# Kernel tuning notes

Measured on AMD Instinct MI355X. Metric: run time of the kernel, lower is better.

Reference implementation:

```python
import jax, jax.numpy as jnp
import numpy as np

N, E, H, G, L = 50000, 640000, 128, 8, 3

def setup_inputs() -> dict:
    key = jax.random.key(0)
    ks = jax.random.split(key, 10)
    s = 1.0 / np.sqrt(H)
    return {
        "x": jax.random.normal(ks[0], (N, H), jnp.float32),
        "query": jax.random.normal(ks[1], (G, H), jnp.float32),
        "Wl": jax.random.normal(ks[2], (L, H, H), jnp.float32) * s,
        "bl": jax.random.normal(ks[3], (L, H), jnp.float32) * s,
        "Wr": jax.random.normal(ks[4], (L, H, H), jnp.float32) * s,
        "Wlin": jax.random.normal(ks[5], (H, H), jnp.float32) * s,
        "blin": jax.random.normal(ks[6], (H,), jnp.float32) * s,
        "edge_index": jax.random.randint(ks[7], (2, E), 0, N, jnp.int64),
        "batch_vec": jnp.sort(jax.random.randint(ks[8], (N,), 0, G, jnp.int64)),
    }

def reference(x, query, Wl, bl, Wr, Wlin, blin, edge_index, batch_vec):
    src, dst = edge_index[0], edge_index[1]
    n = x.shape[0]
    for i in range(L):
        # SAGEConv(aggr='max'): gather neighbor feats, scatter-max to dst
        m = jax.ops.segment_max(x[src], dst, num_segments=n)  # [N,H]
        m = jnp.where(jnp.isfinite(m), m, 0.0)  # isolated nodes -> 0 (PyG)
        x = jax.nn.relu(m @ Wl[i].T + bl[i] + x @ Wr[i].T)
    x = x @ Wlin.T + blin  # encoder final linear
    # cosine scoring per graph, vectorized via batch_vec
    xn = x / jnp.linalg.norm(x, axis=1, keepdims=True).clip(1e-12)
    qn = query / jnp.linalg.norm(query, axis=1, keepdims=True).clip(1e-12)
    scores = jnp.sum(xn * qn[batch_vec], axis=1)  # [N]
    return scores
```

## Files before the change

### kernel.cpp

```cpp
#include <hip/hip_runtime.h>
#include <math.h>

#define H 128
#define NBUCK_MAX 256

typedef _Float16 half8 __attribute__((ext_vector_type(8)));
typedef float f32x16 __attribute__((ext_vector_type(16)));
typedef int int4v __attribute__((ext_vector_type(4)));

__device__ __forceinline__ half8 h8max(half8 a, half8 b) {
#if defined(__has_builtin) && __has_builtin(__builtin_elementwise_max)
    return __builtin_elementwise_max(a, b);
#else
    half8 r;
#pragma unroll
    for (int j = 0; j < 8; ++j) r[j] = a[j] > b[j] ? a[j] : b[j];
    return r;
#endif
}

__device__ __forceinline__ half8 h8shfl_xor(half8 v, int mask) {
    int4v iv;
    __builtin_memcpy(&iv, &v, 16);
#pragma unroll
    for (int j = 0; j < 4; ++j) iv[j] = __shfl_xor(iv[j], mask, 64);
    half8 r;
    __builtin_memcpy(&r, &iv, 16);
    return r;
}


__global__ __launch_bounds__(256) void prep_all(
    const int* __restrict__ ei, int E, int* __restrict__ blockhist, int NB,
    const float* __restrict__ x, const float* __restrict__ query,
    const float* __restrict__ Wl, const float* __restrict__ Wr,
    const float* __restrict__ Wlin, _Float16* __restrict__ xh,
    _Float16* __restrict__ wimg, float* __restrict__ qn, int n8, int HB, int SB,
    int WB) {
    int b = blockIdx.x;
    int tid = threadIdx.x;
    if (b < HB) {
        __shared__ int hist[NBUCK_MAX];
        for (int j = tid; j < NB; j += 256) hist[j] = 0;
        __syncthreads();
        int base = b * 2048 + tid;
#pragma unroll
        for (int k = 0; k < 8; ++k) {
            int e = base + k * 256;
            if (e < E) atomicAdd(&hist[ei[E + e] >> 8], 1);
        }
        __syncthreads();
        for (int j = tid; j < NB; j += 256) blockhist[(size_t)b * NB + j] = hist[j];
    } else if (b < HB + SB) {
        int i = (b - HB) * 256 + tid;
        if (i < n8) {
            const float4* x4 = (const float4*)x;
            float4 u = x4[(size_t)i * 2], v = x4[(size_t)i * 2 + 1];
            float f[8] = {u.x, u.y, u.z, u.w, v.x, v.y, v.z, v.w};
            half8 h;
#pragma unroll
            for (int j = 0; j < 8; ++j) h[j] = (_Float16)f[j];
            *(half8*)(xh + (size_t)i * 8) = h;
        }
    } else if (b < HB + SB + WB) {
        int gidx = (b - HB - SB) * 256 + tid;
        if (gidx < 7 * 2048) {
            int mat = gidx / 2048;
            int rem = gidx - mat * 2048;
            int kc4 = rem >> 9;
            int r2 = rem & 511;
            int s = r2 >> 6;
            int lane = r2 & 63;
            int ks = s >> 2;
            int colgrp = s & 3;
            int lhi = lane >> 5, l31 = lane & 31;
            int n = colgrp * 32 + l31;
            int g16 = kc4 * 4 + ks * 2 + lhi;
            const float* src = (mat == 6) ? Wlin
                             : ((mat & 1) ? Wr + (mat >> 1) * H * H
                                          : Wl + (mat >> 1) * H * H);
            const float* p = src + n * H + g16 * 8;
            half8 h, l;
#pragma unroll
            for (int j = 0; j < 8; ++j) {
                float v = p[j];
                _Float16 hh = (_Float16)v;
                h[j] = hh;
                l[j] = (_Float16)(v - (float)hh);
            }
            size_t base = (size_t)mat * 32768 + (size_t)kc4 * 8192 +
                          (size_t)s * 1024 + (size_t)lane * 16;
            *(half8*)(wimg + base) = h;
            *(half8*)(wimg + base + 8) = l;
        }
    } else {
        int g = b - HB - SB - WB;
        __shared__ float part[4];
        float v = (tid < 128) ? query[g * H + tid] : 0.f;
        float ss = v * v;
#pragma unroll
        for (int off = 32; off > 0; off >>= 1) ss += __shfl_xor(ss, off, 64);
        if ((tid & 63) == 0) part[tid >> 6] = ss;
        __syncthreads();
        float tot = part[0] + part[1];
        if (tid < 128) qn[g * H + tid] = v / fmaxf(sqrtf(tot), 1e-12f);
    }
}


__global__ __launch_bounds__(512) void scan_hist(int* __restrict__ blockhist,
                                                 int HB, int NB,
                                                 int* __restrict__ coltot) {
    __shared__ int buf[512];
    int j = blockIdx.x;
    int tid = threadIdx.x;
    int carry = 0;
    for (int base = 0; base < HB; base += 512) {
        int t = base + tid;
        int v = (t < HB) ? blockhist[(size_t)t * NB + j] : 0;
        buf[tid] = v;
        __syncthreads();
        int incl = v;
#pragma unroll
        for (int off = 1; off < 512; off <<= 1) {
            int u = (tid >= off) ? buf[tid - off] : 0;
            __syncthreads();
            incl += u;
            buf[tid] = incl;
            __syncthreads();
        }
        if (t < HB) blockhist[(size_t)t * NB + j] = carry + incl - v;
        carry += buf[511];
        __syncthreads();
    }
    if (tid == 0) coltot[j] = carry;
}


__global__ __launch_bounds__(256) void scan_buckets(const int* __restrict__ coltot,
                                                    int NB,
                                                    int* __restrict__ colstart) {
    __shared__ int buf[256];
    int tid = threadIdx.x;
    int v = (tid < NB) ? coltot[tid] : 0;
    buf[tid] = v;
    __syncthreads();
    int incl = v;
#pragma unroll
    for (int off = 1; off < 256; off <<= 1) {
        int u = (tid >= off) ? buf[tid - off] : 0;
        __syncthreads();
        incl += u;
        buf[tid] = incl;
        __syncthreads();
    }
    if (tid < NB) colstart[tid] = incl - v;
}


__global__ __launch_bounds__(256) void scatter_edges(
    const int* __restrict__ ei, int E, const int* __restrict__ blockhist,
    const int* __restrict__ colstart, int NB, int2* __restrict__ bucketed) {
    __shared__ int sbase[NBUCK_MAX];
    __shared__ int scnt[NBUCK_MAX];
    int b = blockIdx.x;
    int tid = threadIdx.x;
    for (int j = tid; j < NB; j += 256) {
        sbase[j] = colstart[j] + blockhist[(size_t)b * NB + j];
        scnt[j] = 0;
    }
    __syncthreads();
    int base = b * 2048 + tid;
#pragma unroll
    for (int k = 0; k < 8; ++k) {
        int e = base + k * 256;
        if (e < E) {
            int s = ei[e];
            int d = ei[E + e];
            int bu = d >> 8;
            int r = atomicAdd(&scnt[bu], 1);
            bucketed[sbase[bu] + r] = make_int2(d, s);
        }
    }
}


__global__ __launch_bounds__(256) void build_rows(
    const int2* __restrict__ bucketed, const int* __restrict__ colstart,
    const int* __restrict__ coltot, int* __restrict__ deg,
    int* __restrict__ adjp32, int* __restrict__ govf, int* __restrict__ ovf,
    int N) {
    __shared__ __align__(16) int rows[256 * 32];
    __shared__ int cnt[256];
    int k = blockIdx.x;
    int tid = threadIdx.x;
    cnt[tid] = 0;
    for (int j = tid; j < 256 * 32; j += 256) rows[j] = 0;
    __syncthreads();

    int s0 = colstart[k];
    int cn = coltot[k];
    for (int i = tid; i < cn; i += 256) {
        int2 rec = bucketed[s0 + i];
        int dl = rec.x & 255;
        int sl = atomicAdd(&cnt[dl], 1);
        if (sl < 32) {
            rows[dl * 32 + sl] = rec.y;
        } else {
            int o = atomicAdd(govf, 1);
            ovf[2 * o] = rec.x;
            ovf[2 * o + 1] = rec.y;
        }
    }
    __syncthreads();
    int node0 = k << 8;
    if (node0 + tid < N) deg[node0 + tid] = cnt[tid];
    for (int j = tid; j < 2048; j += 256) {
        int row = j >> 3, q = j & 7;
        int node = node0 + row;
        if (node < N)
            ((int4*)adjp32)[(size_t)node * 8 + q] = ((const int4*)rows)[row * 8 + q];
    }
}


template <bool FINAL_UNUSED>
__global__ __launch_bounds__(512, 8) void layer_fused(
    const half8* __restrict__ Xh, const int* __restrict__ deg,
    const int* __restrict__ adjp32, const int* __restrict__ ovf,
    const int* __restrict__ ovfcnt, const _Float16* __restrict__ Bimg,
    const float* __restrict__ bias, _Float16* __restrict__ Yh, int N) {
    __shared__ __align__(16) unsigned char smem[16384];
    _Float16* sU = (_Float16*)smem;
    _Float16* sX = (_Float16*)(smem + 8192);
    float* comb = (float*)smem;

    int tid = threadIdx.x;
    int w = tid >> 6;
    int wq = w & 3;
    int wh = w >> 2;
    int lane = tid & 63;
    int l31 = lane & 31;
    int lhi = lane >> 5;
    int n0 = blockIdx.x * 32;

    const half8 hz = {(_Float16)0.f, (_Float16)0.f, (_Float16)0.f, (_Float16)0.f,
                      (_Float16)0.f, (_Float16)0.f, (_Float16)0.f, (_Float16)0.f};

    {
        int row = tid >> 4;
        int g = tid & 15;
        int nn = n0 + row;
        half8 h = hz;
        if (nn < N) h = Xh[(size_t)nn * 16 + g];
        *(half8*)&sX[row * 128 + ((g ^ (row & 15)) << 3)] = h;
    }

    {
        int sub = lane >> 4;
        int lf = lane & 15;
        int nd4 = n0 + w * 4;
        int node = nd4 + sub;
        int nodec = node < N ? node : N - 1;
        int degv = (node < N) ? deg[node] : 0;

        int dmx = degv;
        {
            int t = __shfl_xor(dmx, 16, 64);
            dmx = t > dmx ? t : dmx;
            t = __shfl_xor(dmx, 32, 64);
            dmx = t > dmx ? t : dmx;
        }

        int r0 = adjp32[(size_t)nodec * 32 + lf];
        int r1 = 0;
        if (dmx > 16) r1 = adjp32[(size_t)nodec * 32 + 16 + lf];
#pragma unroll
        for (int i = 0; i < 4; ++i) {
            int d = __shfl(degv, i << 4, 64);
            int base = i << 4;
            int j0 = sub, j1 = 4 + sub, j2 = 8 + sub, j3 = 12 + sub;
            int i0 = __shfl(r0, base | (j0 < d ? j0 : 0), 64);
            int i1 = __shfl(r0, base | (j1 < d ? j1 : 0), 64);
            int i2 = __shfl(r0, base | (j2 < d ? j2 : 0), 64);
            int i3 = __shfl(r0, base | (j3 < d ? j3 : 0), 64);
            half8 v0 = Xh[(size_t)i0 * 16 + lf];
            half8 v1 = Xh[(size_t)i1 * 16 + lf];
            half8 v2 = Xh[(size_t)i2 * 16 + lf];
            half8 v3 = Xh[(size_t)i3 * 16 + lf];
            half8 acc = h8max(h8max(v0, v1), h8max(v2, v3));
            if (d > 16) {
                int k4 = (16 + sub) < d ? sub : 0;
                int k5 = (20 + sub) < d ? 4 + sub : 0;
                int k6 = (24 + sub) < d ? 8 + sub : 0;
                int k7 = (28 + sub) < d ? 12 + sub : 0;
                int i4 = __shfl(r1, base | k4, 64);
                int i5 = __shfl(r1, base | k5, 64);
                int i6 = __shfl(r1, base | k6, 64);
                int i7 = __shfl(r1, base | k7, 64);
                half8 u0 = Xh[(size_t)i4 * 16 + lf];
                half8 u1 = Xh[(size_t)i5 * 16 + lf];
                half8 u2 = Xh[(size_t)i6 * 16 + lf];
                half8 u3 = Xh[(size_t)i7 * 16 + lf];
                acc = h8max(acc, h8max(h8max(u0, u1), h8max(u2, u3)));
            }
            if (d > 32) {
                int cntv = ovfcnt[0];
                for (int kk = 0; kk < cntv; ++kk) {
                    if (ovf[2 * kk] == nd4 + i) {
                        half8 u = Xh[(size_t)ovf[2 * kk + 1] * 16 + lf];
                        acc = h8max(acc, u);
                    }
                }
            }
            acc = h8max(acc, h8shfl_xor(acc, 16));
            acc = h8max(acc, h8shfl_xor(acc, 32));
            if (d == 0) acc = hz;
            int row = w * 4 + i;
            if (sub == 0) *(half8*)&sU[row * 128 + ((lf ^ (row & 15)) << 3)] = acc;
        }
    }
    __syncthreads();

    f32x16 acc;
    int col = wq * 32 + l31;
    {
        float b0 = (wh == 0) ? bias[col] : 0.f;
#pragma unroll
        for (int r = 0; r < 16; ++r) acc[r] = b0;
    }

    int rl = l31;
    const _Float16* A = wh ? sX : sU;
    const _Float16* B = Bimg + (size_t)wh * 32768;

#pragma unroll
    for (int kc4 = 0; kc4 < 4; ++kc4) {
#pragma unroll
        for (int ks = 0; ks < 2; ++ks) {
            int g16 = kc4 * 4 + ks * 2 + lhi;
            int posA = g16 ^ (rl & 15);
            half8 ah = *(const half8*)&A[rl * 128 + posA * 8];
            size_t boff =
                (size_t)kc4 * 8192 + (size_t)(ks * 4 + wq) * 1024 + (size_t)lane * 16;
            half8 bh = *(const half8*)&B[boff];
            half8 bl2 = *(const half8*)&B[boff + 8];
            acc = __builtin_amdgcn_mfma_f32_32x32x16_f16(ah, bh, acc, 0, 0, 0);
            acc = __builtin_amdgcn_mfma_f32_32x32x16_f16(ah, bl2, acc, 0, 0, 0);
        }
    }

    __syncthreads();

    if (wh == 1) {
#pragma unroll
        for (int r = 0; r < 16; ++r) {
            int rloc = (r & 3) + 8 * (r >> 2) + 4 * lhi;
            comb[wq * 1024 + rloc * 32 + l31] = acc[r];
        }
    }
    __syncthreads();

    if (wh == 0) {
#pragma unroll
        for (int r = 0; r < 16; ++r) {
            int rloc = (r & 3) + 8 * (r >> 2) + 4 * lhi;
            float y = acc[r] + comb[wq * 1024 + rloc * 32 + l31];
            int row = n0 + rloc;
            if (row < N) Yh[(size_t)row * H + col] = (_Float16)fmaxf(y, 0.f);
        }
    }
}


__global__ __launch_bounds__(256) void final_mfma6(
    const half8* __restrict__ Xh, const _Float16* __restrict__ Bimg,
    const float* __restrict__ blin, const float* __restrict__ qn,
    const int* __restrict__ bv, float* __restrict__ out, int N) {
    __shared__ __align__(16) _Float16 sA[4096];

    int tid = threadIdx.x;
    int w = tid >> 6;
    int lane = tid & 63;
    int l31 = lane & 31;
    int lhi = lane >> 5;
    int n0 = blockIdx.x * 32;

    {
        const half8 hz = {(_Float16)0.f, (_Float16)0.f, (_Float16)0.f, (_Float16)0.f,
                          (_Float16)0.f, (_Float16)0.f, (_Float16)0.f, (_Float16)0.f};
#pragma unroll
        for (int t = 0; t < 2; ++t) {
            int idx = tid + t * 256;
            int row = idx >> 4;
            int g = idx & 15;
            int nn = n0 + row;
            half8 h = hz;
            if (nn < N) h = Xh[(size_t)nn * 16 + g];
            *(half8*)&sA[row * 128 + ((g ^ (row & 15)) << 3)] = h;
        }
    }

    int arow = n0 + l31;
    arow = arow < N ? arow : N - 1;
    int gl = bv[arow];

    f32x16 acc;
    int col = w * 32 + l31;
    {
        float b = blin[col];
#pragma unroll
        for (int r = 0; r < 16; ++r) acc[r] = b;
    }
    int rl = l31;
    __syncthreads();

#pragma unroll
    for (int kc4 = 0; kc4 < 4; ++kc4) {
#pragma unroll
        for (int ks = 0; ks < 2; ++ks) {
            int g16 = kc4 * 4 + ks * 2 + lhi;
            int posA = g16 ^ (rl & 15);
            half8 ah = *(const half8*)&sA[rl * 128 + posA * 8];
            size_t boff =
                (size_t)kc4 * 8192 + (size_t)(ks * 4 + w) * 1024 + (size_t)lane * 16;
            half8 bh = *(const half8*)&Bimg[boff];
            half8 bl2 = *(const half8*)&Bimg[boff + 8];
            acc = __builtin_amdgcn_mfma_f32_32x32x16_f16(ah, bh, acc, 0, 0, 0);
            acc = __builtin_amdgcn_mfma_f32_32x32x16_f16(ah, bl2, acc, 0, 0, 0);
        }
    }

    __syncthreads();
    float* sP = (float*)sA;
#pragma unroll
    for (int r = 0; r < 16; ++r) {
        int rloc = (r & 3) + 8 * (r >> 2) + 4 * lhi;
        int g = __shfl(gl, rloc, 32);
        float y = acc[r];
        float q = qn[(size_t)g * H + col];
        float ss = y * y;
        float sd = y * q;
#pragma unroll
        for (int off = 1; off <= 16; off <<= 1) {
            ss += __shfl_xor(ss, off, 64);
            sd += __shfl_xor(sd, off, 64);
        }
        if (l31 == 0) {
            sP[(rloc * 4 + w) * 2] = ss;
            sP[(rloc * 4 + w) * 2 + 1] = sd;
        }
    }
    __syncthreads();
    if (tid < 32) {
        int row = n0 + tid;
        if (row < N) {
            float ss = 0.f, sd = 0.f;
#pragma unroll
            for (int q = 0; q < 4; ++q) {
                ss += sP[(tid * 4 + q) * 2];
                sd += sP[(tid * 4 + q) * 2 + 1];
            }
            out[row] = sd / fmaxf(sqrtf(ss), 1e-12f);
        }
    }
}


extern "C" void kernel_launch(void* const* d_in, const int* in_sizes, int n_in,
                              void* d_out, int out_size, void* d_ws, size_t ws_size,
                              hipStream_t stream) {
    const float* x = (const float*)d_in[0];
    const float* query = (const float*)d_in[1];
    const float* Wl = (const float*)d_in[2];
    const float* bl = (const float*)d_in[3];
    const float* Wr = (const float*)d_in[4];
    const float* Wlin = (const float*)d_in[5];
    const float* blin = (const float*)d_in[6];
    const int* ei = (const int*)d_in[7];
    const int* bv = (const int*)d_in[8];
    float* out = (float*)d_out;

    const int N = in_sizes[0] / H;
    const int E = in_sizes[7] / 2;
    const int G = in_sizes[1] / H;

    const int HB = (E + 2047) / 2048;
    const int NB = (N + 255) >> 8;

    char* p = (char*)d_ws;
    auto alloc = [&](size_t bytes) {
        char* r = p;
        p += (bytes + 255) & ~(size_t)255;
        return r;
    };
    int* deg = (int*)alloc((size_t)(N + 1) * sizeof(int));
    int* govf = deg + N;
    int* adjp32 = (int*)alloc((size_t)N * 32 * sizeof(int));
    int* ovf = (int*)alloc((size_t)E * 2 * sizeof(int));
    int* blockhist = (int*)alloc((size_t)HB * NB * sizeof(int));
    int* colstart = (int*)alloc((size_t)NB * sizeof(int));
    int* coltot = (int*)alloc((size_t)NB * sizeof(int));
    int2* bucketed = (int2*)alloc((size_t)E * sizeof(int2));
    float* qn = (float*)alloc((size_t)G * H * sizeof(float));
    _Float16* wimg = (_Float16*)alloc((size_t)7 * 32768 * sizeof(_Float16));
    size_t actH = (size_t)N * H * sizeof(_Float16);
    _Float16* xah = (_Float16*)alloc(actH);
    _Float16* xbh = (_Float16*)alloc(actH);

    hipMemsetAsync(govf, 0, sizeof(int), stream);

    const int n8 = N * H / 8;
    const int SB = (n8 + 255) / 256;
    const int WB = (7 * 2048 + 255) / 256;
    prep_all<<<HB + SB + WB + G, 256, 0, stream>>>(ei, E, blockhist, NB, x,
                                                   query, Wl, Wr, Wlin, xah,
                                                   wimg, qn, n8, HB, SB, WB);
    scan_hist<<<NB, 512, 0, stream>>>(blockhist, HB, NB, coltot);
    scan_buckets<<<1, 256, 0, stream>>>(coltot, NB, colstart);
    scatter_edges<<<HB, 256, 0, stream>>>(ei, E, blockhist, colstart, NB,
                                          bucketed);
    build_rows<<<NB, 256, 0, stream>>>(bucketed, colstart, coltot, deg, adjp32,
                                       govf, ovf, N);

    const int NGm = (N + 31) / 32;

    layer_fused<false><<<NGm, 512, 0, stream>>>(
        (const half8*)xah, deg, adjp32, ovf, govf, wimg + (size_t)0 * 65536,
        bl + 0 * H, xbh, N);
    layer_fused<false><<<NGm, 512, 0, stream>>>(
        (const half8*)xbh, deg, adjp32, ovf, govf, wimg + (size_t)1 * 65536,
        bl + 1 * H, xah, N);
    layer_fused<false><<<NGm, 512, 0, stream>>>(
        (const half8*)xah, deg, adjp32, ovf, govf, wimg + (size_t)2 * 65536,
        bl + 2 * H, xbh, N);
    final_mfma6<<<NGm, 256, 0, stream>>>(
        (const half8*)xbh, wimg + (size_t)6 * 32768, blin, qn, bv, out, N);
}
```

Before: 231.4 us.

## Store adjacency as 16-bit indices and fold bucket scan into consumers

The padded adjacency table now holds unsigned short neighbor indices instead of int. This halves the adjacency bytes written by build_rows and read by each layer_fused gather. The separate scan_buckets launch is removed: scatter_edges recomputes the bucket prefix scan in LDS, and build_rows computes its own start offset with a serial loop. The layer kernel's launch bounds occupancy hint also drops from 8 to 6. The 16-bit indices only work when N is below 65536, and every block now repeats the scan work.

New measurement: 233.2 us. Within noise of the previous version (+0.8%).

```diff
diff --git a/kernel.cpp b/kernel.cpp
--- a/kernel.cpp
+++ b/kernel.cpp
@@ -136,12 +136,8 @@
     if (tid == 0) coltot[j] = carry;
 }
 
-
-__global__ __launch_bounds__(256) void scan_buckets(const int* __restrict__ coltot,
-                                                    int NB,
-                                                    int* __restrict__ colstart) {
-    __shared__ int buf[256];
-    int tid = threadIdx.x;
+__device__ __forceinline__ int lds_excl_scan256(const int* __restrict__ coltot,
+                                                int NB, int* buf, int tid) {
     int v = (tid < NB) ? coltot[tid] : 0;
     buf[tid] = v;
     __syncthreads();
@@ -154,20 +150,22 @@
         buf[tid] = incl;
         __syncthreads();
     }
-    if (tid < NB) colstart[tid] = incl - v;
+    return incl - v;
 }
 
 
 __global__ __launch_bounds__(256) void scatter_edges(
     const int* __restrict__ ei, int E, const int* __restrict__ blockhist,
-    const int* __restrict__ colstart, int NB, int2* __restrict__ bucketed) {
+    const int* __restrict__ coltot, int NB, int2* __restrict__ bucketed) {
+    __shared__ int sbuf[256];
     __shared__ int sbase[NBUCK_MAX];
     __shared__ int scnt[NBUCK_MAX];
     int b = blockIdx.x;
     int tid = threadIdx.x;
-    for (int j = tid; j < NB; j += 256) {
-        sbase[j] = colstart[j] + blockhist[(size_t)b * NB + j];
-        scnt[j] = 0;
+    int cs = lds_excl_scan256(coltot, NB, sbuf, tid);
+    if (tid < NB) {
+        sbase[tid] = cs + blockhist[(size_t)b * NB + tid];
+        scnt[tid] = 0;
     }
     __syncthreads();
     int base = b * 2048 + tid;
@@ -186,26 +184,36 @@
 
 
 __global__ __launch_bounds__(256) void build_rows(
-    const int2* __restrict__ bucketed, const int* __restrict__ colstart,
-    const int* __restrict__ coltot, int* __restrict__ deg,
-    int* __restrict__ adjp32, int* __restrict__ govf, int* __restrict__ ovf,
-    int N) {
-    __shared__ __align__(16) int rows[256 * 32];
+    const int2* __restrict__ bucketed, const int* __restrict__ coltot,
+    int NB, int* __restrict__ deg, unsigned short* __restrict__ adjp16,
+    int* __restrict__ govf, int* __restrict__ ovf, int N) {
+    __shared__ int sbuf[256];
+    __shared__ __align__(16) unsigned short rows[256 * 32];
     __shared__ int cnt[256];
     int k = blockIdx.x;
     int tid = threadIdx.x;
+    int cs = lds_excl_scan256(coltot, NB, sbuf, tid);
+    int s0 = __shfl(cs, 0, 64);
+    if (tid == k % 256) sbuf[0] = cs;
+    __syncthreads();
+    if (tid == 0) {
+        int acc = 0;
+        for (int j = 0; j < k; ++j) acc += coltot[j];
+        sbuf[0] = acc;
+        sbuf[1] = coltot[k];
+    }
     cnt[tid] = 0;
     for (int j = tid; j < 256 * 32; j += 256) rows[j] = 0;
     __syncthreads();
-
-    int s0 = colstart[k];
-    int cn = coltot[k];
+    s0 = sbuf[0];
+    int cn = sbuf[1];
+
     for (int i = tid; i < cn; i += 256) {
         int2 rec = bucketed[s0 + i];
         int dl = rec.x & 255;
         int sl = atomicAdd(&cnt[dl], 1);
         if (sl < 32) {
-            rows[dl * 32 + sl] = rec.y;
+            rows[dl * 32 + sl] = (unsigned short)rec.y;
         } else {
             int o = atomicAdd(govf, 1);
             ovf[2 * o] = rec.x;
@@ -215,19 +223,19 @@
     __syncthreads();
     int node0 = k << 8;
     if (node0 + tid < N) deg[node0 + tid] = cnt[tid];
-    for (int j = tid; j < 2048; j += 256) {
-        int row = j >> 3, q = j & 7;
+    for (int j = tid; j < 1024; j += 256) {
+        int row = j >> 2, q = j & 3;
         int node = node0 + row;
         if (node < N)
-            ((int4*)adjp32)[(size_t)node * 8 + q] = ((const int4*)rows)[row * 8 + q];
+            ((int4*)adjp16)[(size_t)node * 4 + q] = ((const int4*)rows)[row * 4 + q];
     }
 }
 
 
 template <bool FINAL_UNUSED>
-__global__ __launch_bounds__(512, 8) void layer_fused(
+__global__ __launch_bounds__(512, 6) void layer_fused(
     const half8* __restrict__ Xh, const int* __restrict__ deg,
-    const int* __restrict__ adjp32, const int* __restrict__ ovf,
+    const unsigned short* __restrict__ adjp16, const int* __restrict__ ovf,
     const int* __restrict__ ovfcnt, const _Float16* __restrict__ Bimg,
     const float* __restrict__ bias, _Float16* __restrict__ Yh, int N) {
     __shared__ __align__(16) unsigned char smem[16384];
@@ -272,9 +280,9 @@
             dmx = t > dmx ? t : dmx;
         }
 
-        int r0 = adjp32[(size_t)nodec * 32 + lf];
+        int r0 = (int)adjp16[(size_t)nodec * 32 + lf];
         int r1 = 0;
-        if (dmx > 16) r1 = adjp32[(size_t)nodec * 32 + 16 + lf];
+        if (dmx > 16) r1 = (int)adjp16[(size_t)nodec * 32 + 16 + lf];
 #pragma unroll
         for (int i = 0; i < 4; ++i) {
             int d = __shfl(degv, i << 4, 64);
@@ -496,10 +504,10 @@
     };
     int* deg = (int*)alloc((size_t)(N + 1) * sizeof(int));
     int* govf = deg + N;
-    int* adjp32 = (int*)alloc((size_t)N * 32 * sizeof(int));
+    unsigned short* adjp16 =
+        (unsigned short*)alloc((size_t)N * 32 * sizeof(unsigned short));
     int* ovf = (int*)alloc((size_t)E * 2 * sizeof(int));
     int* blockhist = (int*)alloc((size_t)HB * NB * sizeof(int));
-    int* colstart = (int*)alloc((size_t)NB * sizeof(int));
     int* coltot = (int*)alloc((size_t)NB * sizeof(int));
     int2* bucketed = (int2*)alloc((size_t)E * sizeof(int2));
     float* qn = (float*)alloc((size_t)G * H * sizeof(float));
@@ -517,22 +525,21 @@
                                                    query, Wl, Wr, Wlin, xah,
                                                    wimg, qn, n8, HB, SB, WB);
     scan_hist<<<NB, 512, 0, stream>>>(blockhist, HB, NB, coltot);
-    scan_buckets<<<1, 256, 0, stream>>>(coltot, NB, colstart);
-    scatter_edges<<<HB, 256, 0, stream>>>(ei, E, blockhist, colstart, NB,
+    scatter_edges<<<HB, 256, 0, stream>>>(ei, E, blockhist, coltot, NB,
                                           bucketed);
-    build_rows<<<NB, 256, 0, stream>>>(bucketed, colstart, coltot, deg, adjp32,
-                                       govf, ovf, N);
+    build_rows<<<NB, 256, 0, stream>>>(bucketed, coltot, NB, deg, adjp16, govf,
+                                       ovf, N);
 
     const int NGm = (N + 31) / 32;
 
     layer_fused<false><<<NGm, 512, 0, stream>>>(
-        (const half8*)xah, deg, adjp32, ovf, govf, wimg + (size_t)0 * 65536,
+        (const half8*)xah, deg, adjp16, ovf, govf, wimg + (size_t)0 * 65536,
         bl + 0 * H, xbh, N);
     layer_fused<false><<<NGm, 512, 0, stream>>>(
-        (const half8*)xbh, deg, adjp32, ovf, govf, wimg + (size_t)1 * 65536,
+        (const half8*)xbh, deg, adjp16, ovf, govf, wimg + (size_t)1 * 65536,
         bl + 1 * H, xah, N);
     layer_fused<false><<<NGm, 512, 0, stream>>>(
-        (const half8*)xah, deg, adjp32, ovf, govf, wimg + (size_t)2 * 65536,
+        (const half8*)xah, deg, adjp16, ovf, govf, wimg + (size_t)2 * 65536,
         bl + 2 * H, xbh, N);
     final_mfma6<<<NGm, 256, 0, stream>>>(
         (const half8*)xbh, wimg + (size_t)6 * 32768, blin, qn, bv, out, N);
```
